# Kernel tuning notes

Measured on AMD Instinct MI355X. Metric: run time of the kernel, lower is better.

Reference implementation:

```python
import jax, jax.numpy as jnp
import numpy as np

S, D, H, DK, DV = 4096, 1024, 16, 64, 64


def setup_inputs() -> dict:
    key = jax.random.key(0)
    ks = jax.random.split(key, 6)
    x = jax.random.normal(ks[0], (S, D), dtype=jnp.float32)
    # per-head projection weights, stacked over heads; scaled for numerical sanity
    Wq = jax.random.normal(ks[1], (H, D, DK), dtype=jnp.float32) / np.sqrt(D)
    Wk = jax.random.normal(ks[2], (H, D, DK), dtype=jnp.float32) / np.sqrt(D)
    Wv = jax.random.normal(ks[3], (H, D, DV), dtype=jnp.float32) / np.sqrt(D)
    Wc = jax.random.normal(ks[4], (H * DV, D), dtype=jnp.float32) / np.sqrt(H * DV)
    bc = jnp.zeros((D,), dtype=jnp.float32)
    return {"x": x, "Wq": Wq, "Wk": Wk, "Wv": Wv, "Wc": Wc, "bc": bc}


def reference(x, Wq, Wk, Wv, Wc, bc):
    # Per-head projections (original loops over heads with separate Linears;
    # stacking over h is the same math, vectorized).
    q = jnp.einsum("sd,hdk->hsk", x, Wq)   # [H,S,DK]
    k = jnp.einsum("sd,hdk->hsk", x, Wk)   # [H,S,DK]
    v = jnp.einsum("sd,hdv->hsv", x, Wv)   # [H,S,DV]
    scores = jnp.einsum("hsk,htk->hst", q, k) / jnp.sqrt(jnp.asarray(DK, x.dtype))
    probs = jax.nn.softmax(scores, axis=-1)  # softmax over last dim, per row
    o = jnp.einsum("hst,htv->hsv", probs, v)  # [H,S,DV]
    cat = jnp.transpose(o, (1, 0, 2)).reshape(S, H * DV)  # concat heads on last dim
    return cat @ Wc + bc  # output projection with bias
```

## Files before the change

kernel.cpp:

```cpp
#include <hip/hip_runtime.h>
#include <hip/hip_bf16.h>

#define S_ 4096
#define D_ 1024
#define H_ 16
#define DK_ 64
#define DV_ 64

typedef short bf16x8 __attribute__((ext_vector_type(8)));
typedef short bf16x4 __attribute__((ext_vector_type(4)));
typedef float floatx4 __attribute__((ext_vector_type(4)));
using bf16 = __hip_bfloat16;

#define MFMA16(a, b, c) __builtin_amdgcn_mfma_f32_16x16x32_bf16(a, b, c, 0, 0, 0)

#if __has_builtin(__builtin_amdgcn_exp2f)
#define EXP2(x) __builtin_amdgcn_exp2f(x)
#else
#define EXP2(x) exp2f(x)
#endif

__device__ __forceinline__ void stage16(const void* g, void* l) {
    __builtin_amdgcn_global_load_lds(
        (const __attribute__((address_space(1))) void*)g,
        (__attribute__((address_space(3))) void*)l, 16, 0, 0);
}

__device__ __forceinline__ bf16x8 ldsfrag(const bf16* base, int row, int chunk) {
    return *(const bf16x8*)(base + row * 64 + (((chunk ^ (row & 7))) << 3));
}
__device__ __forceinline__ bf16x8 ldsfrag32(const bf16* base, int row, int chunk) {
    return *(const bf16x8*)(base + row * 32 + (((chunk ^ (row & 3))) << 3));
}

__device__ __forceinline__ unsigned short bfbits(float f) {
    union { bf16 h; unsigned short u; } c; c.h = __float2bfloat16(f); return c.u;
}
__device__ __forceinline__ float bf2f(bf16 h) { return __bfloat162float(h); }
__device__ __forceinline__ unsigned int pkrne(float lo, float hi) {
    return (unsigned int)bfbits(lo) | ((unsigned int)bfbits(hi) << 16);
}

__device__ __forceinline__ unsigned int pktrunc(float lo, float hi) {
    union { float f; unsigned int u; } a, b;
    a.f = hi; b.f = lo;
    return __builtin_amdgcn_perm(a.u, b.u, 0x07060302u);
}

__global__ __launch_bounds__(256)
void prep(const float* __restrict__ x, const float* __restrict__ Wq,
          const float* __restrict__ Wk, const float* __restrict__ Wv,
          const float* __restrict__ Wc,
          bf16* __restrict__ xb, bf16* __restrict__ Wt, bf16* __restrict__ Wct)
{
    __shared__ float ls[64][65];
    const int bx = blockIdx.x, t = threadIdx.x;

    if (bx < 2048) {
        int i = bx * 2048 + t * 8;
        float4 a = *(const float4*)(x + i);
        float4 b = *(const float4*)(x + i + 4);
        ushort4 lo, hi;
        lo.x = bfbits(a.x); lo.y = bfbits(a.y); lo.z = bfbits(a.z); lo.w = bfbits(a.w);
        hi.x = bfbits(b.x); hi.y = bfbits(b.y); hi.z = bfbits(b.z); hi.w = bfbits(b.w);
        *(ushort4*)(xb + i) = lo;
        *(ushort4*)(xb + i + 4) = hi;
        return;
    }
    if (bx < 2816) {
        const int idx = bx - 2048;
        const int z = idx >> 4, which = z >> 4, h = z & 15;
        const float* s = (which == 0 ? Wq : which == 1 ? Wk : Wv) + (size_t)h * D_ * 64;
        bf16* d = Wt + ((size_t)which * 1024 + h * 64) * D_;
        const float scale = (which == 0) ? 0.125f * 1.44269504088896340736f : 1.0f;
        const int r0 = (idx & 15) * 64;
        {
            int r = t >> 2, cseg = (t & 3) * 16;
            const float* sp = s + (size_t)(r0 + r) * 64 + cseg;
            #pragma unroll
            for (int i = 0; i < 16; i += 4) {
                float4 v = *(const float4*)(sp + i);
                ls[r][cseg + i + 0] = v.x; ls[r][cseg + i + 1] = v.y;
                ls[r][cseg + i + 2] = v.z; ls[r][cseg + i + 3] = v.w;
            }
        }
        __syncthreads();
        {
            int c = t >> 2, rseg = (t & 3) * 16;
            bf16* dp = d + (size_t)c * D_ + r0 + rseg;
            #pragma unroll
            for (int i = 0; i < 16; i++) dp[i] = __float2bfloat16(ls[rseg + i][c] * scale);
        }
        return;
    }
    {
        const int idx = bx - 2816;
        const int r0 = (idx & 15) * 64, c0 = (idx >> 4) * 64;
        {
            int r = t >> 2, cseg = (t & 3) * 16;
            const float* sp = Wc + (size_t)(r0 + r) * D_ + c0 + cseg;
            #pragma unroll
            for (int i = 0; i < 16; i += 4) {
                float4 v = *(const float4*)(sp + i);
                ls[r][cseg + i + 0] = v.x; ls[r][cseg + i + 1] = v.y;
                ls[r][cseg + i + 2] = v.z; ls[r][cseg + i + 3] = v.w;
            }
        }
        __syncthreads();
        {
            int c = t >> 2, rseg = (t & 3) * 16;
            bf16* dp = Wct + (size_t)(c0 + c) * D_ + r0 + rseg;
            #pragma unroll
            for (int i = 0; i < 16; i++) dp[i] = __float2bfloat16(ls[rseg + i][c]);
        }
    }
}

__global__ __launch_bounds__(256)
void qkv_gemm(const bf16* __restrict__ xb, const bf16* __restrict__ Wt,
              bf16* __restrict__ Qb, bf16* __restrict__ Kb, bf16* __restrict__ Vtb)
{
    const int m0 = blockIdx.x * 128;
    const int n0 = blockIdx.y * 128;
    __shared__ __align__(16) bf16 xa[2][128 * 32];
    __shared__ __align__(16) bf16 wb2[2][128 * 32];

    const int t = threadIdx.x, lane = t & 63, w = t >> 6;
    const int l15 = lane & 15, quad = lane >> 4;

    auto stage_a = [&](int buf, int kk) {
        #pragma unroll
        for (int j = 0; j < 2; j++) {
            int row = j * 64 + (t >> 2);
            int ch  = (t & 3) ^ (row & 3);
            stage16((const char*)xb + ((size_t)(m0 + row) * D_ + kk) * 2 + ch * 16,
                    (char*)&xa[buf][0] + (j * 4 + w) * 1024);
        }
    };
    auto stage_b = [&](int buf, int kk) {
        #pragma unroll
        for (int j = 0; j < 2; j++) {
            int row = j * 64 + (t >> 2);
            int ch  = (t & 3) ^ (row & 3);
            stage16((const char*)Wt + ((size_t)(n0 + row) * D_ + kk) * 2 + ch * 16,
                    (char*)&wb2[buf][0] + (j * 4 + w) * 1024);
        }
    };

    const floatx4 fz = {0.f, 0.f, 0.f, 0.f};
    floatx4 acc[2][8];
    #pragma unroll
    for (int mt = 0; mt < 2; mt++)
        #pragma unroll
        for (int nt = 0; nt < 8; nt++) acc[mt][nt] = fz;

    const int which = n0 >> 10;

    stage_a(0, 0); stage_b(0, 0);
    if (which != 2) {
        for (int kt = 0; kt < 32; kt++) {
            int cur = kt & 1;
            __syncthreads();
            if (kt < 31) { stage_a(cur ^ 1, (kt + 1) * 32); stage_b(cur ^ 1, (kt + 1) * 32); }
            bf16x8 a0 = ldsfrag32(&xa[cur][0], w * 32 + l15,      quad);
            bf16x8 a1 = ldsfrag32(&xa[cur][0], w * 32 + 16 + l15, quad);
            #pragma unroll
            for (int nt = 0; nt < 8; nt++) {
                bf16x8 b = ldsfrag32(&wb2[cur][0], nt * 16 + l15, quad);
                acc[0][nt] = MFMA16(b, a0, acc[0][nt]);
                acc[1][nt] = MFMA16(b, a1, acc[1][nt]);
            }
        }
        bf16* base = (which == 0) ? Qb : Kb;
        #pragma unroll
        for (int nt = 0; nt < 8; nt++) {
            int n  = n0 + nt * 16 + quad * 4;
            int hh = (n >> 6) & 15, col = n & 63;
            #pragma unroll
            for (int mt = 0; mt < 2; mt++) {
                int s = m0 + w * 32 + mt * 16 + l15;
                uint2 o;
                o.x = pkrne(acc[mt][nt][0], acc[mt][nt][1]);
                o.y = pkrne(acc[mt][nt][2], acc[mt][nt][3]);
                *(uint2*)(base + ((size_t)hh * S_ + s) * 64 + col) = o;
            }
        }
    } else {
        for (int kt = 0; kt < 32; kt++) {
            int cur = kt & 1;
            __syncthreads();
            if (kt < 31) { stage_a(cur ^ 1, (kt + 1) * 32); stage_b(cur ^ 1, (kt + 1) * 32); }
            bf16x8 a0 = ldsfrag32(&xa[cur][0], w * 32 + l15,      quad);
            bf16x8 a1 = ldsfrag32(&xa[cur][0], w * 32 + 16 + l15, quad);
            #pragma unroll
            for (int nt = 0; nt < 8; nt++) {
                bf16x8 b = ldsfrag32(&wb2[cur][0], nt * 16 + l15, quad);
                acc[0][nt] = MFMA16(a0, b, acc[0][nt]);
                acc[1][nt] = MFMA16(a1, b, acc[1][nt]);
            }
        }
        #pragma unroll
        for (int nt = 0; nt < 8; nt++) {
            int n = n0 + nt * 16 + l15;
            int hh = (n >> 6) & 15, col = n & 63;
            #pragma unroll
            for (int mt = 0; mt < 2; mt++) {
                int s = m0 + w * 32 + mt * 16 + quad * 4;
                uint2 o;
                o.x = pkrne(acc[mt][nt][0], acc[mt][nt][1]);
                o.y = pkrne(acc[mt][nt][2], acc[mt][nt][3]);
                *(uint2*)(Vtb + ((size_t)hh * 64 + col) * S_ + s) = o;
            }
        }
    }
}

template<int NKT, bool FULL>
__global__ __attribute__((amdgpu_waves_per_eu(4, 4))) __launch_bounds__(256)
void attn(const bf16* __restrict__ Qb, const bf16* __restrict__ Kb,
          const bf16* __restrict__ Vtb, bf16* __restrict__ Cat,
          bf16* __restrict__ Opart, float* __restrict__ lpart)
{
    const int m0 = blockIdx.x * 128;
    const int h  = blockIdx.y;
    const int half = blockIdx.z;
    const int keybase = half * (NKT * 64);

    __shared__ __align__(16) bf16 ka[2][64 * 64];
    __shared__ __align__(16) bf16 vt[2][64 * 64];

    const int t = threadIdx.x, lane = t & 63, w = t >> 6;
    const int l15 = lane & 15, quad = lane >> 4;

    auto stage_kv = [&](int buf, int key0) {
        const char* kg = (const char*)(Kb + ((size_t)h * S_ + key0) * 64);
        #pragma unroll
        for (int j = 0; j < 2; j++) {
            int c = (j * 4 + w) * 64 + lane;
            int row = c >> 3, ch = (c & 7) ^ (row & 7);
            stage16(kg + row * 128 + ch * 16, (char*)&ka[buf][0] + (j * 4 + w) * 1024);
        }
        const char* vg = (const char*)(Vtb + (size_t)h * 64 * S_ + key0);
        #pragma unroll
        for (int j = 0; j < 2; j++) {
            int c = (j * 4 + w) * 64 + lane;
            int row = c >> 3, ch = (c & 7) ^ (row & 7);
            stage16(vg + (size_t)row * (S_ * 2) + ch * 16, (char*)&vt[buf][0] + (j * 4 + w) * 1024);
        }
    };

    bf16x8 qf[2][2];
    #pragma unroll
    for (int nq = 0; nq < 2; nq++)
        #pragma unroll
        for (int ks = 0; ks < 2; ks++)
            qf[nq][ks] = *(const bf16x8*)(Qb +
                ((size_t)h * S_ + m0 + w * 32 + nq * 16 + l15) * 64 + ks * 32 + quad * 8);

    const floatx4 fz = {0.f, 0.f, 0.f, 0.f};
    floatx4 acc[2][4];
    float rs[2] = {0.f, 0.f};
    #pragma unroll
    for (int nq = 0; nq < 2; nq++)
        #pragma unroll
        for (int nt = 0; nt < 4; nt++) acc[nq][nt] = fz;

    stage_kv(0, keybase);
    __syncthreads();

    for (int kt = 0; kt < NKT; kt++) {
        const int cur = kt & 1;
        if (kt + 1 < NKT) stage_kv(cur ^ 1, keybase + (kt + 1) * 64);

        floatx4 sc[4][2];
        #pragma unroll
        for (int mk = 0; mk < 4; mk++)
            #pragma unroll
            for (int nq = 0; nq < 2; nq++) sc[mk][nq] = fz;
        #pragma unroll
        for (int ks = 0; ks < 2; ks++) {
            bf16x8 af[4];
            #pragma unroll
            for (int mk = 0; mk < 4; mk++)
                af[mk] = ldsfrag(&ka[cur][0], mk * 16 + l15, ks * 4 + quad);
            #pragma unroll
            for (int mk = 0; mk < 4; mk++)
                #pragma unroll
                for (int nq = 0; nq < 2; nq++)
                    sc[mk][nq] = MFMA16(af[mk], qf[nq][ks], sc[mk][nq]);
        }

        union bf4u { bf16x4 v; unsigned int u[2]; };
        bf4u pf[4][2];
        #pragma unroll
        for (int mk = 0; mk < 4; mk++)
            #pragma unroll
            for (int nq = 0; nq < 2; nq++) {
                float p0 = EXP2(sc[mk][nq][0]);
                float p1 = EXP2(sc[mk][nq][1]);
                float p2 = EXP2(sc[mk][nq][2]);
                float p3 = EXP2(sc[mk][nq][3]);
                rs[nq] += (p0 + p1) + (p2 + p3);
                pf[mk][nq].u[0] = pktrunc(p0, p1);
                pf[mk][nq].u[1] = pktrunc(p2, p3);
            }

        #pragma unroll
        for (int p = 0; p < 2; p++) {
            union { bf16x8 v8; bf16x4 v4[2]; } b8[2];
            #pragma unroll
            for (int nq = 0; nq < 2; nq++) {
                b8[nq].v4[0] = pf[2 * p + 0][nq].v;
                b8[nq].v4[1] = pf[2 * p + 1][nq].v;
            }
            #pragma unroll
            for (int nt = 0; nt < 4; nt++) {
                const char* vb = (const char*)&vt[cur][0]
                               + (nt * 16 + l15) * 128 + (quad & 1) * 8;
                const int r7 = l15 & 7;
                union { bf16x8 v8; bf16x4 v4[2]; } a8;
                a8.v4[0] = *(const bf16x4*)(vb + (((4 * p +     (quad >> 1)) ^ r7) << 4));
                a8.v4[1] = *(const bf16x4*)(vb + (((4 * p + 2 + (quad >> 1)) ^ r7) << 4));
                #pragma unroll
                for (int nq = 0; nq < 2; nq++)
                    acc[nq][nt] = MFMA16(a8.v8, b8[nq].v8, acc[nq][nt]);
            }
        }
        __syncthreads();
    }

    #pragma unroll
    for (int nq = 0; nq < 2; nq++) {
        rs[nq] += __shfl_xor(rs[nq], 16);
        rs[nq] += __shfl_xor(rs[nq], 32);
    }

    if (FULL) {
        #pragma unroll
        for (int nq = 0; nq < 2; nq++) {
            float inv = 1.0f / rs[nq];
            int q = m0 + w * 32 + nq * 16 + l15;
            #pragma unroll
            for (int nt = 0; nt < 4; nt++) {
                uint2 o;
                o.x = pktrunc(acc[nq][nt][0] * inv, acc[nq][nt][1] * inv);
                o.y = pktrunc(acc[nq][nt][2] * inv, acc[nq][nt][3] * inv);
                *(uint2*)(Cat + (size_t)q * (H_ * DV_) + h * 64 + nt * 16 + quad * 4) = o;
            }
        }
    } else {
        const size_t plane = (size_t)(half * H_ + h) * S_;
        #pragma unroll
        for (int nq = 0; nq < 2; nq++) {
            int q = m0 + w * 32 + nq * 16 + l15;
            #pragma unroll
            for (int nt = 0; nt < 4; nt++) {
                uint2 o;
                o.x = pktrunc(acc[nq][nt][0], acc[nq][nt][1]);
                o.y = pktrunc(acc[nq][nt][2], acc[nq][nt][3]);
                *(uint2*)(Opart + (plane + q) * 64 + nt * 16 + quad * 4) = o;
            }
            if (quad == 0) lpart[plane + q] = rs[nq];
        }
    }
}

__global__ __launch_bounds__(256)
void combine(const bf16* __restrict__ Opart, const float* __restrict__ lpart,
             bf16* __restrict__ Cat)
{
    const int h = blockIdx.y;
    const int off = (blockIdx.x * 256 + threadIdx.x) * 8;
    const int s = off >> 6, dv = off & 63;
    union { bf16x8 v; bf16 e[8]; } o0, o1;
    o0.v = *(const bf16x8*)(Opart + (size_t)h * S_ * 64 + off);
    o1.v = *(const bf16x8*)(Opart + (size_t)(H_ + h) * S_ * 64 + off);
    float inv = 1.0f / (lpart[(size_t)h * S_ + s] + lpart[(size_t)(H_ + h) * S_ + s]);
    uint4 o;
    o.x = pktrunc((bf2f(o0.e[0]) + bf2f(o1.e[0])) * inv, (bf2f(o0.e[1]) + bf2f(o1.e[1])) * inv);
    o.y = pktrunc((bf2f(o0.e[2]) + bf2f(o1.e[2])) * inv, (bf2f(o0.e[3]) + bf2f(o1.e[3])) * inv);
    o.z = pktrunc((bf2f(o0.e[4]) + bf2f(o1.e[4])) * inv, (bf2f(o0.e[5]) + bf2f(o1.e[5])) * inv);
    o.w = pktrunc((bf2f(o0.e[6]) + bf2f(o1.e[6])) * inv, (bf2f(o0.e[7]) + bf2f(o1.e[7])) * inv);
    *(uint4*)(Cat + (size_t)s * (H_ * DV_) + h * 64 + dv) = o;
}

__global__ __launch_bounds__(256)
void out_proj(const bf16* __restrict__ Cat, const bf16* __restrict__ Wct,
              const float* __restrict__ bc, float* __restrict__ out)
{
    const int m0 = blockIdx.x * 128;
    const int n0 = blockIdx.y * 64;
    __shared__ __align__(16) bf16 ca[2][128 * 32];
    __shared__ __align__(16) bf16 wb2[2][64 * 32];

    const int t = threadIdx.x, lane = t & 63, w = t >> 6;
    const int l15 = lane & 15, quad = lane >> 4;

    auto stage_a = [&](int buf, int kk) {
        #pragma unroll
        for (int j = 0; j < 2; j++) {
            int row = j * 64 + (t >> 2);
            int ch  = (t & 3) ^ (row & 3);
            stage16((const char*)Cat + ((size_t)(m0 + row) * D_ + kk) * 2 + ch * 16,
                    (char*)&ca[buf][0] + (j * 4 + w) * 1024);
        }
    };
    auto stage_b = [&](int buf, int kk) {
        int row = t >> 2;
        int ch  = (t & 3) ^ (row & 3);
        stage16((const char*)Wct + ((size_t)(n0 + row) * D_ + kk) * 2 + ch * 16,
                (char*)&wb2[buf][0] + w * 1024);
    };

    const floatx4 fz = {0.f, 0.f, 0.f, 0.f};
    floatx4 acc[2][4];
    #pragma unroll
    for (int mt = 0; mt < 2; mt++)
        #pragma unroll
        for (int nt = 0; nt < 4; nt++) acc[mt][nt] = fz;

    stage_a(0, 0); stage_b(0, 0);
    for (int kt = 0; kt < 32; kt++) {
        int cur = kt & 1;
        __syncthreads();
        if (kt < 31) { stage_a(cur ^ 1, (kt + 1) * 32); stage_b(cur ^ 1, (kt + 1) * 32); }
        bf16x8 a0 = ldsfrag32(&ca[cur][0], w * 32 + l15,      quad);
        bf16x8 a1 = ldsfrag32(&ca[cur][0], w * 32 + 16 + l15, quad);
        #pragma unroll
        for (int nt = 0; nt < 4; nt++) {
            bf16x8 b = ldsfrag32(&wb2[cur][0], nt * 16 + l15, quad);
            acc[0][nt] = MFMA16(a0, b, acc[0][nt]);
            acc[1][nt] = MFMA16(a1, b, acc[1][nt]);
        }
    }

    #pragma unroll
    for (int nt = 0; nt < 4; nt++) {
        int col = n0 + nt * 16 + l15;
        float bias = bc[col];
        #pragma unroll
        for (int mt = 0; mt < 2; mt++)
            #pragma unroll
            for (int r = 0; r < 4; r++) {
                int row = m0 + w * 32 + mt * 16 + quad * 4 + r;
                out[(size_t)row * D_ + col] = acc[mt][nt][r] + bias;
            }
    }
}

extern "C" void kernel_launch(void* const* d_in, const int* in_sizes, int n_in,
                              void* d_out, int out_size, void* d_ws, size_t ws_size,
                              hipStream_t stream)
{
    const float* x  = (const float*)d_in[0];
    const float* Wq = (const float*)d_in[1];
    const float* Wk = (const float*)d_in[2];
    const float* Wv = (const float*)d_in[3];
    const float* Wc = (const float*)d_in[4];
    const float* bc = (const float*)d_in[5];
    float* out = (float*)d_out;

    bf16* xb  = (bf16*)d_ws;
    bf16* Cat = xb;
    bf16* Wt  = xb  + (size_t)S_ * D_;
    bf16* Wct = Wt  + (size_t)3 * H_ * 64 * D_;
    bf16* Qb  = Wct + (size_t)D_ * H_ * DV_;
    bf16* Kb  = Qb  + (size_t)H_ * S_ * 64;
    bf16* Vtb = Kb  + (size_t)H_ * S_ * 64;
    bf16* Opart = Vtb + (size_t)H_ * 64 * S_;
    float* lpart = (float*)(Opart + (size_t)2 * H_ * S_ * 64);

    const size_t need_split = (size_t)((char*)(lpart + (size_t)2 * H_ * S_) - (char*)d_ws);
    const bool split = ws_size >= need_split;

    prep<<<dim3(3072), 256, 0, stream>>>(x, Wq, Wk, Wv, Wc, xb, Wt, Wct);
    qkv_gemm<<<dim3(S_ / 128, 3072 / 128), 256, 0, stream>>>(xb, Wt, Qb, Kb, Vtb);

    if (split) {
        attn<32, false><<<dim3(S_ / 128, H_, 2), 256, 0, stream>>>(
            Qb, Kb, Vtb, Cat, Opart, lpart);
        combine<<<dim3(S_ * 64 / 2048, H_), 256, 0, stream>>>(Opart, lpart, Cat);
    } else {
        attn<64, true><<<dim3(S_ / 128, H_, 1), 256, 0, stream>>>(
            Qb, Kb, Vtb, Cat, Opart, lpart);
    }

    out_proj<<<dim3(S_ / 128, D_ / 64), 256, 0, stream>>>(Cat, Wct, bc, out);
}
```

Baseline: 234.2 us.

## Split attention keys into four parts with single-buffered LDS kernel

Adds an attention kernel that splits the key range into four parts instead of two and uses single-buffered K/V LDS tiles with an extra barrier per step. It also drops the waves_per_eu attribute. Halving LDS per block and doubling the grid is meant to raise occupancy and improve load balance across CUs. The cost is lost load/compute overlap within a block, twice the partial-output traffic, and a heavier combine pass.

```diff
diff --git a/kernel.cpp b/kernel.cpp
--- a/kernel.cpp
+++ b/kernel.cpp
@@ -40,7 +40,6 @@
 __device__ __forceinline__ unsigned int pkrne(float lo, float hi) {
     return (unsigned int)bfbits(lo) | ((unsigned int)bfbits(hi) << 16);
 }
-
 __device__ __forceinline__ unsigned int pktrunc(float lo, float hi) {
     union { float f; unsigned int u; } a, b;
     a.f = hi; b.f = lo;
@@ -215,6 +214,150 @@
     }
 }
 
+struct AttnState {
+    bf16x8 qf[2][2];
+    floatx4 acc[2][4];
+    float rs[2];
+};
+
+__device__ __forceinline__ void attn_iter(AttnState& st, const bf16* ka,
+                                          const bf16* vt, int l15, int quad)
+{
+    const floatx4 fz = {0.f, 0.f, 0.f, 0.f};
+    floatx4 sc[4][2];
+    #pragma unroll
+    for (int mk = 0; mk < 4; mk++)
+        #pragma unroll
+        for (int nq = 0; nq < 2; nq++) sc[mk][nq] = fz;
+    #pragma unroll
+    for (int ks = 0; ks < 2; ks++) {
+        bf16x8 af[4];
+        #pragma unroll
+        for (int mk = 0; mk < 4; mk++)
+            af[mk] = ldsfrag(ka, mk * 16 + l15, ks * 4 + quad);
+        #pragma unroll
+        for (int mk = 0; mk < 4; mk++)
+            #pragma unroll
+            for (int nq = 0; nq < 2; nq++)
+                sc[mk][nq] = MFMA16(af[mk], st.qf[nq][ks], sc[mk][nq]);
+    }
+
+    union bf4u { bf16x4 v; unsigned int u[2]; };
+    bf4u pf[4][2];
+    #pragma unroll
+    for (int mk = 0; mk < 4; mk++)
+        #pragma unroll
+        for (int nq = 0; nq < 2; nq++) {
+            float p0 = EXP2(sc[mk][nq][0]);
+            float p1 = EXP2(sc[mk][nq][1]);
+            float p2 = EXP2(sc[mk][nq][2]);
+            float p3 = EXP2(sc[mk][nq][3]);
+            st.rs[nq] += (p0 + p1) + (p2 + p3);
+            pf[mk][nq].u[0] = pktrunc(p0, p1);
+            pf[mk][nq].u[1] = pktrunc(p2, p3);
+        }
+
+    #pragma unroll
+    for (int p = 0; p < 2; p++) {
+        union { bf16x8 v8; bf16x4 v4[2]; } b8[2];
+        #pragma unroll
+        for (int nq = 0; nq < 2; nq++) {
+            b8[nq].v4[0] = pf[2 * p + 0][nq].v;
+            b8[nq].v4[1] = pf[2 * p + 1][nq].v;
+        }
+        #pragma unroll
+        for (int nt = 0; nt < 4; nt++) {
+            const char* vb = (const char*)vt + (nt * 16 + l15) * 128 + (quad & 1) * 8;
+            const int r7 = l15 & 7;
+            union { bf16x8 v8; bf16x4 v4[2]; } a8;
+            a8.v4[0] = *(const bf16x4*)(vb + (((4 * p +     (quad >> 1)) ^ r7) << 4));
+            a8.v4[1] = *(const bf16x4*)(vb + (((4 * p + 2 + (quad >> 1)) ^ r7) << 4));
+            #pragma unroll
+            for (int nq = 0; nq < 2; nq++)
+                st.acc[nq][nt] = MFMA16(a8.v8, b8[nq].v8, st.acc[nq][nt]);
+        }
+    }
+}
+
+template<int NKT>
+__global__ __launch_bounds__(256)
+void attn_sb(const bf16* __restrict__ Qb, const bf16* __restrict__ Kb,
+             const bf16* __restrict__ Vtb,
+             bf16* __restrict__ Opart, float* __restrict__ lpart)
+{
+    const int m0 = blockIdx.x * 128;
+    const int h  = blockIdx.y;
+    const int part = blockIdx.z;
+    const int keybase = part * (NKT * 64);
+
+    __shared__ __align__(16) bf16 ka[64 * 64];
+    __shared__ __align__(16) bf16 vt[64 * 64];
+
+    const int t = threadIdx.x, lane = t & 63, w = t >> 6;
+    const int l15 = lane & 15, quad = lane >> 4;
+
+    auto stage_kv = [&](int key0) {
+        const char* kg = (const char*)(Kb + ((size_t)h * S_ + key0) * 64);
+        #pragma unroll
+        for (int j = 0; j < 2; j++) {
+            int c = (j * 4 + w) * 64 + lane;
+            int row = c >> 3, ch = (c & 7) ^ (row & 7);
+            stage16(kg + row * 128 + ch * 16, (char*)&ka[0] + (j * 4 + w) * 1024);
+        }
+        const char* vg = (const char*)(Vtb + (size_t)h * 64 * S_ + key0);
+        #pragma unroll
+        for (int j = 0; j < 2; j++) {
+            int c = (j * 4 + w) * 64 + lane;
+            int row = c >> 3, ch = (c & 7) ^ (row & 7);
+            stage16(vg + (size_t)row * (S_ * 2) + ch * 16, (char*)&vt[0] + (j * 4 + w) * 1024);
+        }
+    };
+
+    AttnState st;
+    const floatx4 fz = {0.f, 0.f, 0.f, 0.f};
+    st.rs[0] = st.rs[1] = 0.f;
+    #pragma unroll
+    for (int nq = 0; nq < 2; nq++) {
+        #pragma unroll
+        for (int nt = 0; nt < 4; nt++) st.acc[nq][nt] = fz;
+        #pragma unroll
+        for (int ks = 0; ks < 2; ks++)
+            st.qf[nq][ks] = *(const bf16x8*)(Qb +
+                ((size_t)h * S_ + m0 + w * 32 + nq * 16 + l15) * 64 + ks * 32 + quad * 8);
+    }
+
+    stage_kv(keybase);
+    __syncthreads();
+    for (int kt = 0; kt < NKT; kt++) {
+        attn_iter(st, ka, vt, l15, quad);
+        if (kt + 1 < NKT) {
+            __syncthreads();
+            stage_kv(keybase + (kt + 1) * 64);
+            __syncthreads();
+        }
+    }
+
+    #pragma unroll
+    for (int nq = 0; nq < 2; nq++) {
+        st.rs[nq] += __shfl_xor(st.rs[nq], 16);
+        st.rs[nq] += __shfl_xor(st.rs[nq], 32);
+    }
+
+    const size_t plane = (size_t)(part * H_ + h) * S_;
+    #pragma unroll
+    for (int nq = 0; nq < 2; nq++) {
+        int q = m0 + w * 32 + nq * 16 + l15;
+        #pragma unroll
+        for (int nt = 0; nt < 4; nt++) {
+            uint2 o;
+            o.x = pktrunc(st.acc[nq][nt][0], st.acc[nq][nt][1]);
+            o.y = pktrunc(st.acc[nq][nt][2], st.acc[nq][nt][3]);
+            *(uint2*)(Opart + (plane + q) * 64 + nt * 16 + quad * 4) = o;
+        }
+        if (quad == 0) lpart[plane + q] = st.rs[nq];
+    }
+}
+
 template<int NKT, bool FULL>
 __global__ __attribute__((amdgpu_waves_per_eu(4, 4))) __launch_bounds__(256)
 void attn(const bf16* __restrict__ Qb, const bf16* __restrict__ Kb,
@@ -249,21 +392,18 @@
         }
     };
 
-    bf16x8 qf[2][2];
-    #pragma unroll
-    for (int nq = 0; nq < 2; nq++)
+    AttnState st;
+    const floatx4 fz = {0.f, 0.f, 0.f, 0.f};
+    st.rs[0] = st.rs[1] = 0.f;
+    #pragma unroll
+    for (int nq = 0; nq < 2; nq++) {
+        #pragma unroll
+        for (int nt = 0; nt < 4; nt++) st.acc[nq][nt] = fz;
         #pragma unroll
         for (int ks = 0; ks < 2; ks++)
-            qf[nq][ks] = *(const bf16x8*)(Qb +
+            st.qf[nq][ks] = *(const bf16x8*)(Qb +
                 ((size_t)h * S_ + m0 + w * 32 + nq * 16 + l15) * 64 + ks * 32 + quad * 8);
-
-    const floatx4 fz = {0.f, 0.f, 0.f, 0.f};
-    floatx4 acc[2][4];
-    float rs[2] = {0.f, 0.f};
-    #pragma unroll
-    for (int nq = 0; nq < 2; nq++)
-        #pragma unroll
-        for (int nt = 0; nt < 4; nt++) acc[nq][nt] = fz;
+    }
 
     stage_kv(0, keybase);
     __syncthreads();
@@ -271,80 +411,26 @@
     for (int kt = 0; kt < NKT; kt++) {
         const int cur = kt & 1;
         if (kt + 1 < NKT) stage_kv(cur ^ 1, keybase + (kt + 1) * 64);
-
-        floatx4 sc[4][2];
-        #pragma unroll
-        for (int mk = 0; mk < 4; mk++)
-            #pragma unroll
-            for (int nq = 0; nq < 2; nq++) sc[mk][nq] = fz;
-        #pragma unroll
-        for (int ks = 0; ks < 2; ks++) {
-            bf16x8 af[4];
-            #pragma unroll
-            for (int mk = 0; mk < 4; mk++)
-                af[mk] = ldsfrag(&ka[cur][0], mk * 16 + l15, ks * 4 + quad);
-            #pragma unroll
-            for (int mk = 0; mk < 4; mk++)
-                #pragma unroll
-                for (int nq = 0; nq < 2; nq++)
-                    sc[mk][nq] = MFMA16(af[mk], qf[nq][ks], sc[mk][nq]);
-        }
-
-        union bf4u { bf16x4 v; unsigned int u[2]; };
-        bf4u pf[4][2];
-        #pragma unroll
-        for (int mk = 0; mk < 4; mk++)
-            #pragma unroll
-            for (int nq = 0; nq < 2; nq++) {
-                float p0 = EXP2(sc[mk][nq][0]);
-                float p1 = EXP2(sc[mk][nq][1]);
-                float p2 = EXP2(sc[mk][nq][2]);
-                float p3 = EXP2(sc[mk][nq][3]);
-                rs[nq] += (p0 + p1) + (p2 + p3);
-                pf[mk][nq].u[0] = pktrunc(p0, p1);
-                pf[mk][nq].u[1] = pktrunc(p2, p3);
-            }
-
-        #pragma unroll
-        for (int p = 0; p < 2; p++) {
-            union { bf16x8 v8; bf16x4 v4[2]; } b8[2];
-            #pragma unroll
-            for (int nq = 0; nq < 2; nq++) {
-                b8[nq].v4[0] = pf[2 * p + 0][nq].v;
-                b8[nq].v4[1] = pf[2 * p + 1][nq].v;
-            }
-            #pragma unroll
-            for (int nt = 0; nt < 4; nt++) {
-                const char* vb = (const char*)&vt[cur][0]
-                               + (nt * 16 + l15) * 128 + (quad & 1) * 8;
-                const int r7 = l15 & 7;
-                union { bf16x8 v8; bf16x4 v4[2]; } a8;
-                a8.v4[0] = *(const bf16x4*)(vb + (((4 * p +     (quad >> 1)) ^ r7) << 4));
-                a8.v4[1] = *(const bf16x4*)(vb + (((4 * p + 2 + (quad >> 1)) ^ r7) << 4));
-                #pragma unroll
-                for (int nq = 0; nq < 2; nq++)
-                    acc[nq][nt] = MFMA16(a8.v8, b8[nq].v8, acc[nq][nt]);
-            }
-        }
+        attn_iter(st, &ka[cur][0], &vt[cur][0], l15, quad);
         __syncthreads();
     }
 
     #pragma unroll
     for (int nq = 0; nq < 2; nq++) {
-        rs[nq] += __shfl_xor(rs[nq], 16);
-        rs[nq] += __shfl_xor(rs[nq], 32);
+        st.rs[nq] += __shfl_xor(st.rs[nq], 16);
+        st.rs[nq] += __shfl_xor(st.rs[nq], 32);
     }
 
     if (FULL) {
         #pragma unroll
         for (int nq = 0; nq < 2; nq++) {
-            float inv = 1.0f / rs[nq];
+            float inv = 1.0f / st.rs[nq];
             int q = m0 + w * 32 + nq * 16 + l15;
             #pragma unroll
             for (int nt = 0; nt < 4; nt++) {
                 uint2 o;
-                o.x = pktrunc(acc[nq][nt][0] * inv, acc[nq][nt][1] * inv);
-                o.y = pktrunc(acc[nq][nt][2] * inv, acc[nq][nt][3] * inv);
+                o.x = pktrunc(st.acc[nq][nt][0] * inv, st.acc[nq][nt][1] * inv);
+                o.y = pktrunc(st.acc[nq][nt][2] * inv, st.acc[nq][nt][3] * inv);
                 *(uint2*)(Cat + (size_t)q * (H_ * DV_) + h * 64 + nt * 16 + quad * 4) = o;
             }
         }
@@ -356,15 +442,16 @@
             #pragma unroll
             for (int nt = 0; nt < 4; nt++) {
                 uint2 o;
-                o.x = pktrunc(acc[nq][nt][0], acc[nq][nt][1]);
-                o.y = pktrunc(acc[nq][nt][2], acc[nq][nt][3]);
+                o.x = pktrunc(st.acc[nq][nt][0], st.acc[nq][nt][1]);
+                o.y = pktrunc(st.acc[nq][nt][2], st.acc[nq][nt][3]);
                 *(uint2*)(Opart + (plane + q) * 64 + nt * 16 + quad * 4) = o;
             }
-            if (quad == 0) lpart[plane + q] = rs[nq];
-        }
-    }
-}
-
+            if (quad == 0) lpart[plane + q] = st.rs[nq];
+        }
+    }
+}
+
+template<int PARTS>
 __global__ __launch_bounds__(256)
 void combine(const bf16* __restrict__ Opart, const float* __restrict__ lpart,
              bf16* __restrict__ Cat)
@@ -372,16 +459,23 @@
     const int h = blockIdx.y;
     const int off = (blockIdx.x * 256 + threadIdx.x) * 8;
     const int s = off >> 6, dv = off & 63;
-    union { bf16x8 v; bf16 e[8]; } o0, o1;
-    o0.v = *(const bf16x8*)(Opart + (size_t)h * S_ * 64 + off);
-    o1.v = *(const bf16x8*)(Opart + (size_t)(H_ + h) * S_ * 64 + off);
-    float inv = 1.0f / (lpart[(size_t)h * S_ + s] + lpart[(size_t)(H_ + h) * S_ + s]);
-    uint4 o;
-    o.x = pktrunc((bf2f(o0.e[0]) + bf2f(o1.e[0])) * inv, (bf2f(o0.e[1]) + bf2f(o1.e[1])) * inv);
-    o.y = pktrunc((bf2f(o0.e[2]) + bf2f(o1.e[2])) * inv, (bf2f(o0.e[3]) + bf2f(o1.e[3])) * inv);
-    o.z = pktrunc((bf2f(o0.e[4]) + bf2f(o1.e[4])) * inv, (bf2f(o0.e[5]) + bf2f(o1.e[5])) * inv);
-    o.w = pktrunc((bf2f(o0.e[6]) + bf2f(o1.e[6])) * inv, (bf2f(o0.e[7]) + bf2f(o1.e[7])) * inv);
-    *(uint4*)(Cat + (size_t)s * (H_ * DV_) + h * 64 + dv) = o;
+    float o[8] = {0, 0, 0, 0, 0, 0, 0, 0};
+    float lsum = 0.f;
+    #pragma unroll
+    for (int p = 0; p < PARTS; p++) {
+        union { bf16x8 v; bf16 e[8]; } ov;
+        ov.v = *(const bf16x8*)(Opart + (size_t)(p * H_ + h) * S_ * 64 + off);
+        #pragma unroll
+        for (int i = 0; i < 8; i++) o[i] += bf2f(ov.e[i]);
+        lsum += lpart[(size_t)(p * H_ + h) * S_ + s];
+    }
+    float inv = 1.0f / lsum;
+    uint4 ou;
+    ou.x = pktrunc(o[0] * inv, o[1] * inv);
+    ou.y = pktrunc(o[2] * inv, o[3] * inv);
+    ou.z = pktrunc(o[4] * inv, o[5] * inv);
+    ou.w = pktrunc(o[6] * inv, o[7] * inv);
+    *(uint4*)(Cat + (size_t)s * (H_ * DV_) + h * 64 + dv) = ou;
 }
 
 __global__ __launch_bounds__(256)
@@ -468,21 +562,26 @@
     bf16* Kb  = Qb  + (size_t)H_ * S_ * 64;
     bf16* Vtb = Kb  + (size_t)H_ * S_ * 64;
     bf16* Opart = Vtb + (size_t)H_ * 64 * S_;
-    float* lpart = (float*)(Opart + (size_t)2 * H_ * S_ * 64);
-
-    const size_t need_split = (size_t)((char*)(lpart + (size_t)2 * H_ * S_) - (char*)d_ws);
-    const bool split = ws_size >= need_split;
+    float* lpart4 = (float*)(Opart + (size_t)4 * H_ * S_ * 64);
+    float* lpart2 = (float*)(Opart + (size_t)2 * H_ * S_ * 64);
+
+    const size_t need4 = (size_t)((char*)(lpart4 + (size_t)4 * H_ * S_) - (char*)d_ws);
+    const size_t need2 = (size_t)((char*)(lpart2 + (size_t)2 * H_ * S_) - (char*)d_ws);
 
     prep<<<dim3(3072), 256, 0, stream>>>(x, Wq, Wk, Wv, Wc, xb, Wt, Wct);
     qkv_gemm<<<dim3(S_ / 128, 3072 / 128), 256, 0, stream>>>(xb, Wt, Qb, Kb, Vtb);
 
-    if (split) {
+    if (ws_size >= need4) {
+        attn_sb<16><<<dim3(S_ / 128, H_, 4), 256, 0, stream>>>(
+            Qb, Kb, Vtb, Opart, lpart4);
+        combine<4><<<dim3(S_ * 64 / 2048, H_), 256, 0, stream>>>(Opart, lpart4, Cat);
+    } else if (ws_size >= need2) {
         attn<32, false><<<dim3(S_ / 128, H_, 2), 256, 0, stream>>>(
-            Qb, Kb, Vtb, Cat, Opart, lpart);
-        combine<<<dim3(S_ * 64 / 2048, H_), 256, 0, stream>>>(Opart, lpart, Cat);
+            Qb, Kb, Vtb, Cat, Opart, lpart2);
+        combine<2><<<dim3(S_ * 64 / 2048, H_), 256, 0, stream>>>(Opart, lpart2, Cat);
     } else {
         attn<64, true><<<dim3(S_ / 128, H_, 1), 256, 0, stream>>>(
-            Qb, Kb, Vtb, Cat, Opart, lpart);
+            Qb, Kb, Vtb, Cat, Opart, lpart2);
     }
 
     out_proj<<<dim3(S_ / 128, D_ / 64), 256, 0, stream>>>(Cat, Wct, bc, out);
```

New measurement: 248.5 us. 1.06x slower.
